# Performance work log

Hardware: AMD Instinct MI355X
Metric: run time of the kernel (lower is better)

The kernel has to match this reference:

```python
import jax, jax.numpy as jnp
import numpy as np

B, T, H = 4, 4096, 1024


def setup_inputs() -> dict:
    key = jax.random.key(0)
    ks = jax.random.split(key, 10)
    W_STD = 0.02  # small init keeps the WKV denominator well-conditioned
    inp = {
        "x": jax.random.normal(ks[0], (B, T, H), dtype=jnp.float32),
        "time_decay": jnp.exp(-jax.random.uniform(ks[1], (H,), minval=0.5, maxval=1.5)),
        "time_mix_key": jax.random.uniform(ks[2], (H,)),
        "time_mix_value": jax.random.uniform(ks[3], (H,)),
        "time_mix_receptance": jax.random.uniform(ks[4], (H,)),
        "W_receptance": jax.random.normal(ks[5], (H, H)) * W_STD,
        "W_key": jax.random.normal(ks[6], (H, H)) * W_STD,
        "W_value": jax.random.normal(ks[7], (H, H)) * W_STD,
        "W_out": jax.random.normal(ks[8], (H, H)) * W_STD,
        "b_out": jax.random.normal(ks[9], (H,)) * W_STD,
    }
    return inp


def reference(x, time_decay, time_mix_key, time_mix_value, time_mix_receptance,
              W_receptance, W_key, W_value, W_out, b_out):
    # time_shift: shifted[:, t] = x[:, t-1], shifted[:, 0] = 0
    shifted = jnp.pad(x, ((0, 0), (1, 0), (0, 0)))[:, :-1]
    xs = x + shifted  # original applies SAME mix to x and shifted
    k = (xs * time_mix_key) @ W_key.T          # [B,T,H]
    v = (xs * time_mix_value) @ W_value.T      # [B,T,H]
    r = jax.nn.sigmoid((xs * time_mix_receptance) @ W_receptance.T)

    def step(carry, kv):
        num, den = carry                       # [B,H] each
        ck, cv = kv                            # [B,H]
        out = (num + time_decay * ck * den) / (den + time_decay * ck)
        ek = jnp.exp(ck)
        return (time_decay * num + ek * cv, time_decay * den + ek), out

    init = (jnp.ones_like(k[:, 0]), jnp.ones_like(k[:, 0]))
    kT = jnp.swapaxes(k, 0, 1)  # [T,B,H]
    vT = jnp.swapaxes(v, 0, 1)
    _, outT = jax.lax.scan(step, init, (kT, vT))
    out = jnp.swapaxes(outT, 0, 1)             # [B,T,H]
    return (r * out) @ W_out.T + b_out
```

## Files before the change

### kernel.cpp

```cpp
#include <hip/hip_runtime.h>

#define H_DIM 1024
#define T_DIM 4096
#define B_DIM 4
#define M_DIM (B_DIM * T_DIM)
#define SCAN_C 32
#define SCAN_W 48

typedef __attribute__((ext_vector_type(8))) short short8;
typedef __attribute__((ext_vector_type(4))) float f32x4;
typedef _Float16 half8 __attribute__((ext_vector_type(8)));

__device__ __forceinline__ unsigned short f2h(float f) {
  _Float16 h = (_Float16)f;
  return __builtin_bit_cast(unsigned short, h);
}
__device__ __forceinline__ float h2f(unsigned short u) {
  return (float)__builtin_bit_cast(_Float16, u);
}

__device__ __forceinline__ double fast_exp64(double x) {
  const double L2E = 1.4426950408889634074;
  const double LN2 = 0.69314718055994530942;
  double z = x * L2E;
  double n = rint(z);
  double y = (z - n) * LN2;
  double p = 2.7557319223985890653e-6;
  p = fma(p, y, 2.4801587301587301566e-5);
  p = fma(p, y, 1.9841269841269841253e-4);
  p = fma(p, y, 1.3888888888888889419e-3);
  p = fma(p, y, 8.3333333333333332177e-3);
  p = fma(p, y, 4.1666666666666664354e-2);
  p = fma(p, y, 1.6666666666666665741e-1);
  p = fma(p, y, 0.5);
  p = fma(p, y, 1.0);
  p = fma(p, y, 1.0);
  long long bits = ((long long)(1023 + (int)n)) << 52;
  return p * __longlong_as_double(bits);
}

__global__ void prep_kernel(const float* __restrict__ x,
                            const float* __restrict__ Wrec, const float* __restrict__ Wkey,
                            const float* __restrict__ Wval, const float* __restrict__ Wout,
                            const float* __restrict__ tmk, const float* __restrict__ tmv,
                            const float* __restrict__ tmr,
                            unsigned short* __restrict__ xs1, unsigned short* __restrict__ xs2,
                            unsigned short* __restrict__ WK1H, unsigned short* __restrict__ WK2H,
                            unsigned short* __restrict__ WVRH, unsigned short* __restrict__ WOH) {
  int bid = blockIdx.x;
  if (bid < 16384) {
    int i = bid * 256 + threadIdx.x;
    const int HV = H_DIM / 4;
    int m = i / HV;
    int t = m & (T_DIM - 1);
    float4 cur = reinterpret_cast<const float4*>(x)[i];
    float4 prev = make_float4(0.f, 0.f, 0.f, 0.f);
    if (t > 0) prev = reinterpret_cast<const float4*>(x)[i - HV];
    float s[4] = {cur.x + prev.x, cur.y + prev.y, cur.z + prev.z, cur.w + prev.w};
    unsigned short a1[4], a2[4];
#pragma unroll
    for (int q = 0; q < 4; ++q) {
      unsigned short h1 = f2h(s[q]);
      a1[q] = h1;
      a2[q] = f2h((s[q] - h2f(h1)) * 2048.0f);
    }
    reinterpret_cast<ushort4*>(xs1)[i] = make_ushort4(a1[0], a1[1], a1[2], a1[3]);
    reinterpret_cast<ushort4*>(xs2)[i] = make_ushort4(a2[0], a2[1], a2[2], a2[3]);
  } else {
    int i = (bid - 16384) * 256 + threadIdx.x;
    int j = i & (H_DIM - 1);
    float wk = Wkey[i] * tmk[j];
    unsigned short k1 = f2h(wk);
    WK1H[i] = k1;
    WK2H[i] = f2h((wk - h2f(k1)) * 2048.0f);
    WVRH[i] = f2h(Wval[i] * tmv[j]);
    WVRH[H_DIM * H_DIM + i] = f2h(Wrec[i] * tmr[j]);
    WOH[i] = f2h(Wout[i]);
  }
}

#define GBAR() do { asm volatile("" ::: "memory"); __builtin_amdgcn_sched_barrier(0); \
                    __builtin_amdgcn_s_barrier(); \
                    __builtin_amdgcn_sched_barrier(0); asm volatile("" ::: "memory"); } while (0)
#define WAIT_VM6() asm volatile("s_waitcnt vmcnt(6)" ::: "memory")
#define WAIT_VM3() asm volatile("s_waitcnt vmcnt(3)" ::: "memory")
#define WAIT_VM0() asm volatile("s_waitcnt vmcnt(0)" ::: "memory")

__device__ __forceinline__ f32x4 mma_h(short8 a, short8 b, f32x4 c) {
  return __builtin_amdgcn_mfma_f32_16x16x32_f16(
      __builtin_bit_cast(half8, a), __builtin_bit_cast(half8, b), c, 0, 0, 0);
}

__device__ __forceinline__ void stage_r128(const unsigned short* base, int rowoff, int kt,
                                           unsigned dst, int wid, int lane,
                                           unsigned char* smem) {
  int row = wid * 16 + (lane >> 2);
  int col8 = (lane & 3) ^ ((row >> 1) & 3);
  const unsigned short* src = base + (size_t)(rowoff + row) * 1024 + kt * 32 + col8 * 8;
  __builtin_amdgcn_global_load_lds(
      (const __attribute__((address_space(1))) void*)src,
      (__attribute__((address_space(3))) void*)(smem + dst + wid * 1024), 16, 0, 0);
}
__device__ __forceinline__ void stage_r256(const unsigned short* base, int rowoff, int kt,
                                           unsigned dst, int wid, int lane,
                                           unsigned char* smem) {
#pragma unroll
  for (int i = 0; i < 2; ++i) {
    int row = wid * 32 + i * 16 + (lane >> 2);
    int col8 = (lane & 3) ^ ((row >> 1) & 3);
    const unsigned short* src = base + (size_t)(rowoff + row) * 1024 + kt * 32 + col8 * 8;
    __builtin_amdgcn_global_load_lds(
        (const __attribute__((address_space(1))) void*)src,
        (__attribute__((address_space(3))) void*)(smem + dst + wid * 2048 + i * 1024), 16, 0, 0);
  }
}
__device__ __forceinline__ short8 frag_ld2(const unsigned char* smem, unsigned rbase,
                                           int row, int kg) {
  return *reinterpret_cast<const short8*>(smem + rbase + row * 64 + ((kg ^ ((row >> 1) & 3)) * 16));
}

__device__ void gemm_k_body(const unsigned short* __restrict__ A1,
                            const unsigned short* __restrict__ A2,
                            const unsigned short* __restrict__ B1,
                            const unsigned short* __restrict__ B2,
                            float* __restrict__ C, int bid, unsigned char* smem) {
  const int tid = threadIdx.x;
  const int wid = tid >> 6;
  const int lane = tid & 63;
  const int wm = wid >> 2;
  const int wn = wid & 3;
  const int frow = lane & 15;
  const int kg = lane >> 4;
  const int swz = (bid & 7) * 64 + (bid >> 3);
  const int brow = (swz >> 2) << 7;
  const int bcol = (swz & 3) << 8;

  f32x4 acc0[4][4], acc1[4][4];
#pragma unroll
  for (int f = 0; f < 4; ++f)
#pragma unroll
    for (int c = 0; c < 4; ++c) {
      acc0[f][c] = (f32x4){0.f, 0.f, 0.f, 0.f};
      acc1[f][c] = (f32x4){0.f, 0.f, 0.f, 0.f};
    }

  const int NT = 32;
#pragma unroll
  for (int t0 = 0; t0 < 2; ++t0) {
    unsigned sb = t0 * 49152u;
    stage_r128(A1, brow, t0, sb + 0u, wid, lane, smem);
    stage_r128(A2, brow, t0, sb + 8192u, wid, lane, smem);
    stage_r256(B1, bcol, t0, sb + 16384u, wid, lane, smem);
    stage_r256(B2, bcol, t0, sb + 32768u, wid, lane, smem);
  }
  WAIT_VM6();
  GBAR();

  for (int t = 0; t < NT; ++t) {
    unsigned sb = (unsigned)(t % 3) * 49152u;
    unsigned st = (unsigned)((t + 2) % 3) * 49152u;
    const bool stg = (t + 2 < NT);
    short8 a1[4], a2[4], b1[4], b2[4];
#pragma unroll
    for (int f = 0; f < 4; ++f) a1[f] = frag_ld2(smem, sb + 0u, wm * 64 + f * 16 + frow, kg);
#pragma unroll
    for (int c = 0; c < 4; ++c) b1[c] = frag_ld2(smem, sb + 16384u, wn * 64 + c * 16 + frow, kg);
    if (stg) {
      stage_r128(A1, brow, t + 2, st + 0u, wid, lane, smem);
      stage_r128(A2, brow, t + 2, st + 8192u, wid, lane, smem);
    }
    GBAR();
    __builtin_amdgcn_s_setprio(1);
#pragma unroll
    for (int f = 0; f < 4; ++f)
#pragma unroll
      for (int c = 0; c < 4; ++c)
        acc0[f][c] = mma_h(a1[f], b1[c], acc0[f][c]);
    __builtin_amdgcn_s_setprio(0);
    GBAR();
#pragma unroll
    for (int c = 0; c < 4; ++c) b2[c] = frag_ld2(smem, sb + 32768u, wn * 64 + c * 16 + frow, kg);
#pragma unroll
    for (int f = 0; f < 4; ++f) a2[f] = frag_ld2(smem, sb + 8192u, wm * 64 + f * 16 + frow, kg);
    if (stg) {
      stage_r256(B1, bcol, t + 2, st + 16384u, wid, lane, smem);
      stage_r256(B2, bcol, t + 2, st + 32768u, wid, lane, smem);
      WAIT_VM6();
    } else {
      WAIT_VM0();
    }
    GBAR();
    __builtin_amdgcn_s_setprio(1);
#pragma unroll
    for (int f = 0; f < 4; ++f)
#pragma unroll
      for (int c = 0; c < 4; ++c)
        acc1[f][c] = mma_h(a1[f], b2[c], acc1[f][c]);
#pragma unroll
    for (int f = 0; f < 4; ++f)
#pragma unroll
      for (int c = 0; c < 4; ++c)
        acc1[f][c] = mma_h(a2[f], b1[c], acc1[f][c]);
    __builtin_amdgcn_s_setprio(0);
    GBAR();
  }
  WAIT_VM0();

#pragma unroll
  for (int f = 0; f < 4; ++f) {
    int r0 = brow + wm * 64 + f * 16 + kg * 4;
#pragma unroll
    for (int c = 0; c < 4; ++c) {
      int cc = bcol + wn * 64 + c * 16 + frow;
#pragma unroll
      for (int q = 0; q < 4; ++q)
        C[(size_t)(r0 + q) * H_DIM + cc] =
            fmaf(0.00048828125f, acc1[f][c][q], acc0[f][c][q]);
    }
  }
}

__device__ __forceinline__ void stage_half(const unsigned short* base, int rowoff,
                                           int ktp, int kk, int slot,
                                           int wid, int lane, unsigned char* smem) {
#pragma unroll
  for (int i = 0; i < 2; ++i) {
    int row = wid * 32 + i * 16 + (lane >> 2);
    int kcol8 = (lane & 3) ^ ((row >> 1) & 3);
    const unsigned short* src = base + (size_t)(rowoff + row) * 1024
                                + ktp * 64 + kk * 32 + kcol8 * 8;
    unsigned int doff = (unsigned int)(slot * 16384 + wid * 2048 + i * 1024);
    __builtin_amdgcn_global_load_lds(
        (const __attribute__((address_space(1))) void*)src,
        (__attribute__((address_space(3))) void*)(smem + doff), 16, 0, 0);
  }
}
__device__ __forceinline__ short8 frag_ld(const unsigned char* smem, int slot, int row, int kg) {
  int byte = slot * 16384 + row * 64 + ((kg ^ ((row >> 1) & 3)) * 16);
  return *reinterpret_cast<const short8*>(smem + byte);
}

__device__ void gemm_vr_body(const unsigned short* __restrict__ Ag,
                             const unsigned short* __restrict__ Bg,
                             unsigned short* __restrict__ C, int bid,
                             unsigned char* smem) {
  const int tid = threadIdx.x;
  const int wid = tid >> 6;
  const int lane = tid & 63;
  const int wm = wid >> 2;
  const int wn = wid & 3;
  const int frow = lane & 15;
  const int kg = lane >> 4;
  const int swz = (bid & 7) * 64 + (bid >> 3);
  const int brow = (swz >> 3) << 8;
  const int bcol = (swz & 7) << 8;

  f32x4 acc[8][4];
#pragma unroll
  for (int f = 0; f < 8; ++f)
#pragma unroll
    for (int c = 0; c < 4; ++c)
      acc[f][c] = (f32x4){0.f, 0.f, 0.f, 0.f};

  const int NT = 16;
  stage_half(Ag, brow, 0, 0, 0, wid, lane, smem);
  stage_half(Bg, bcol, 0, 0, 1, wid, lane, smem);
  stage_half(Ag, brow, 0, 1, 2, wid, lane, smem);
  stage_half(Bg, bcol, 0, 1, 3, wid, lane, smem);
  stage_half(Ag, brow, 1, 0, 4, wid, lane, smem);
  stage_half(Bg, bcol, 1, 0, 5, wid, lane, smem);
  stage_half(Ag, brow, 1, 1, 6, wid, lane, smem);
  WAIT_VM6();
  GBAR();

  for (int t = 0; t < NT; ++t) {
    const int cur4 = (t & 1) * 4;
    const int nxt4 = cur4 ^ 4;
    short8 a[4], b[4];
#pragma unroll
    for (int f = 0; f < 4; ++f) a[f] = frag_ld(smem, cur4 + 0, wm * 128 + f * 16 + frow, kg);
#pragma unroll
    for (int c = 0; c < 4; ++c) b[c] = frag_ld(smem, cur4 + 1, wn * 64 + c * 16 + frow, kg);
    if (t + 1 < NT) stage_half(Bg, bcol, t + 1, 1, nxt4 + 3, wid, lane, smem);
    GBAR();
    __builtin_amdgcn_s_setprio(1);
#pragma unroll
    for (int f = 0; f < 4; ++f)
#pragma unroll
      for (int c = 0; c < 4; ++c)
        acc[f][c] = mma_h(a[f], b[c], acc[f][c]);
    __builtin_amdgcn_s_setprio(0);
    GBAR();
#pragma unroll
    for (int f = 0; f < 4; ++f) a[f] = frag_ld(smem, cur4 + 0, wm * 128 + (f + 4) * 16 + frow, kg);
    if (t + 2 < NT) stage_half(Ag, brow, t + 2, 0, cur4 + 0, wid, lane, smem);
    GBAR();
    __builtin_amdgcn_s_setprio(1);
#pragma unroll
    for (int f = 0; f < 4; ++f)
#pragma unroll
      for (int c = 0; c < 4; ++c)
        acc[f + 4][c] = mma_h(a[f], b[c], acc[f + 4][c]);
    __builtin_amdgcn_s_setprio(0);
    GBAR();
#pragma unroll
    for (int f = 0; f < 4; ++f) a[f] = frag_ld(smem, cur4 + 2, wm * 128 + f * 16 + frow, kg);
#pragma unroll
    for (int c = 0; c < 4; ++c) b[c] = frag_ld(smem, cur4 + 3, wn * 64 + c * 16 + frow, kg);
    if (t + 2 < NT) stage_half(Bg, bcol, t + 2, 0, cur4 + 1, wid, lane, smem);
    GBAR();
    __builtin_amdgcn_s_setprio(1);
#pragma unroll
    for (int f = 0; f < 4; ++f)
#pragma unroll
      for (int c = 0; c < 4; ++c)
        acc[f][c] = mma_h(a[f], b[c], acc[f][c]);
    __builtin_amdgcn_s_setprio(0);
    GBAR();
#pragma unroll
    for (int f = 0; f < 4; ++f) a[f] = frag_ld(smem, cur4 + 2, wm * 128 + (f + 4) * 16 + frow, kg);
    if (t + 2 < NT) stage_half(Ag, brow, t + 2, 1, cur4 + 2, wid, lane, smem);
    if (t + 2 < NT) { WAIT_VM6(); } else { WAIT_VM0(); }
    GBAR();
    __builtin_amdgcn_s_setprio(1);
#pragma unroll
    for (int f = 0; f < 4; ++f)
#pragma unroll
      for (int c = 0; c < 4; ++c)
        acc[f + 4][c] = mma_h(a[f], b[c], acc[f + 4][c]);
    __builtin_amdgcn_s_setprio(0);
    GBAR();
  }
  WAIT_VM0();

#pragma unroll
  for (int f = 0; f < 8; ++f) {
    int r0 = brow + wm * 128 + f * 16 + kg * 4;
#pragma unroll
    for (int c = 0; c < 4; ++c) {
      int cc = bcol + wn * 64 + c * 16 + frow;
#pragma unroll
      for (int q = 0; q < 4; ++q)
        C[(size_t)(r0 + q) * 2048 + cc] = f2h(acc[f][c][q]);
    }
  }
}

__global__ __launch_bounds__(512, 2) void front_kernel(
    const unsigned short* __restrict__ XS1, const unsigned short* __restrict__ XS2,
    const unsigned short* __restrict__ WK1, const unsigned short* __restrict__ WK2,
    const unsigned short* __restrict__ WVR,
    float* __restrict__ Ck, unsigned short* __restrict__ Cvr) {
  __shared__ __attribute__((aligned(16))) unsigned char smem[147456];
  int bid = blockIdx.x;
  if (bid < 512)
    gemm_k_body(XS1, XS2, WK1, WK2, Ck, bid, smem);
  else
    gemm_vr_body(XS1, WVR, Cvr, bid - 512, smem);
}

__global__ __launch_bounds__(512, 4) void gemm_o_kernel(const unsigned short* __restrict__ Ag,
                                                        const unsigned short* __restrict__ Bg,
                                                        float* __restrict__ C,
                                                        const float* __restrict__ bias) {
  __shared__ __attribute__((aligned(16))) unsigned char smem[73728];
  const int tid = threadIdx.x;
  const int wid = tid >> 6;
  const int lane = tid & 63;
  const int wm = wid >> 2;
  const int wn = wid & 3;
  const int frow = lane & 15;
  const int kg = lane >> 4;
  const int bid = blockIdx.x;
  const int swz = (bid & 7) * 64 + (bid >> 3);
  const int brow = (swz >> 2) << 7;
  const int bcol = (swz & 3) << 8;

  f32x4 acc[4][4];
#pragma unroll
  for (int f = 0; f < 4; ++f)
#pragma unroll
    for (int c = 0; c < 4; ++c)
      acc[f][c] = (f32x4){0.f, 0.f, 0.f, 0.f};

  const int NT = 32;
#pragma unroll
  for (int t0 = 0; t0 < 2; ++t0) {
    unsigned sb = t0 * 24576u;
    stage_r128(Ag, brow, t0, sb + 0u, wid, lane, smem);
    stage_r256(Bg, bcol, t0, sb + 8192u, wid, lane, smem);
  }
  WAIT_VM3();
  GBAR();

  for (int t = 0; t < NT; ++t) {
    unsigned sb = (unsigned)(t % 3) * 24576u;
    unsigned st = (unsigned)((t + 2) % 3) * 24576u;
    const bool stg = (t + 2 < NT);
    short8 a[4], b[4];
#pragma unroll
    for (int f = 0; f < 4; ++f) a[f] = frag_ld2(smem, sb + 0u, wm * 64 + f * 16 + frow, kg);
#pragma unroll
    for (int c = 0; c < 4; ++c) b[c] = frag_ld2(smem, sb + 8192u, wn * 64 + c * 16 + frow, kg);
    if (stg) {
      stage_r128(Ag, brow, t + 2, st + 0u, wid, lane, smem);
      stage_r256(Bg, bcol, t + 2, st + 8192u, wid, lane, smem);
      WAIT_VM3();
    } else {
      WAIT_VM0();
    }
    GBAR();
    __builtin_amdgcn_s_setprio(1);
#pragma unroll
    for (int f = 0; f < 4; ++f)
#pragma unroll
      for (int c = 0; c < 4; ++c)
        acc[f][c] = mma_h(a[f], b[c], acc[f][c]);
    __builtin_amdgcn_s_setprio(0);
    GBAR();
  }
  WAIT_VM0();

#pragma unroll
  for (int f = 0; f < 4; ++f) {
    int r0 = brow + wm * 64 + f * 16 + kg * 4;
#pragma unroll
    for (int c = 0; c < 4; ++c) {
      int cc = bcol + wn * 64 + c * 16 + frow;
      float bb = bias[cc];
#pragma unroll
      for (int q = 0; q < 4; ++q)
        C[(size_t)(r0 + q) * H_DIM + cc] = acc[f][c][q] + bb;
    }
  }
}

__global__ void wkv_scan_kernel(const float* __restrict__ kbuf,
                                const unsigned short* __restrict__ vrbuf,
                                const float* __restrict__ tdec,
                                unsigned short* __restrict__ rwh) {
  const int h = (blockIdx.x * 64 + threadIdx.x) * 2;
  const int chunk = blockIdx.y;
  const int b = blockIdx.z;
  const int t0 = chunk * SCAN_C;
  int tstart = t0 - SCAN_W;
  if (tstart < 0) tstart = 0;
  const int tend = t0 + SCAN_C;
  double num0, den0, num1, den1;
  if (tstart == 0) { num0 = num1 = 1.0; den0 = den1 = 1.0; }
  else             { num0 = num1 = 0.0; den0 = den1 = 0.0; }
  const double w0 = (double)tdec[h];
  const double w1 = (double)tdec[h + 1];
  size_t ik = ((size_t)b * T_DIM + tstart) * H_DIM + h;
  size_t iv = ((size_t)b * T_DIM + tstart) * 2048 + h;
  float2 kc = *reinterpret_cast<const float2*>(kbuf + ik);
  unsigned int vc = *reinterpret_cast<const unsigned int*>(vrbuf + iv);
  unsigned int rc = *reinterpret_cast<const unsigned int*>(vrbuf + iv + 1024);
  for (int t = tstart; t < tend; ++t) {
    size_t adv = (t + 1 < tend) ? 1 : 0;
    float2 kn = *reinterpret_cast<const float2*>(kbuf + ik + adv * H_DIM);
    unsigned int vn = *reinterpret_cast<const unsigned int*>(vrbuf + iv + adv * 2048);
    unsigned int rn = *reinterpret_cast<const unsigned int*>(vrbuf + iv + adv * 2048 + 1024);
    double ck0 = (double)kc.x, ck1 = (double)kc.y;
    if (t >= t0) {
      double p0 = w0 * ck0, p1 = w1 * ck1;
      float o0 = (float)fma(p0, den0, num0) / (float)(den0 + p0);
      float o1 = (float)fma(p1, den1, num1) / (float)(den1 + p1);
      float rr0 = 1.0f / (1.0f + __expf(-h2f((unsigned short)(rc & 0xffffu))));
      float rr1 = 1.0f / (1.0f + __expf(-h2f((unsigned short)(rc >> 16))));
      unsigned int wout = (unsigned int)f2h(rr0 * o0) | ((unsigned int)f2h(rr1 * o1) << 16);
      *reinterpret_cast<unsigned int*>(rwh + ik) = wout;
    }
    double ek0 = fast_exp64(ck0);
    double ek1 = fast_exp64(ck1);
    num0 = fma(w0, num0, ek0 * (double)h2f((unsigned short)(vc & 0xffffu)));
    den0 = fma(w0, den0, ek0);
    num1 = fma(w1, num1, ek1 * (double)h2f((unsigned short)(vc >> 16)));
    den1 = fma(w1, den1, ek1);
    kc = kn; vc = vn; rc = rn;
    ik += H_DIM; iv += 2048;
  }
}

extern "C" void kernel_launch(void* const* d_in, const int* in_sizes, int n_in,
                              void* d_out, int out_size, void* d_ws, size_t ws_size,
                              hipStream_t stream) {
  const float* x    = (const float*)d_in[0];
  const float* tdec = (const float*)d_in[1];
  const float* tmk  = (const float*)d_in[2];
  const float* tmv  = (const float*)d_in[3];
  const float* tmr  = (const float*)d_in[4];
  const float* Wrec = (const float*)d_in[5];
  const float* Wkey = (const float*)d_in[6];
  const float* Wval = (const float*)d_in[7];
  const float* Wout = (const float*)d_in[8];
  const float* bout = (const float*)d_in[9];
  float* out = (float*)d_out;
  unsigned char* ws = (unsigned char*)d_ws;

  const size_t W2 = (size_t)H_DIM * H_DIM * 2;
  const size_t BF_FULL = (size_t)M_DIM * H_DIM * 2;
  const size_t NEED = 2 * BF_FULL + 2 * BF_FULL + 5 * W2;
  if (ws_size < NEED) return;

  size_t off = 0;
  unsigned short* XS1H = (unsigned short*)(ws + off); off += BF_FULL;
  unsigned short* XS2H = (unsigned short*)(ws + off); off += BF_FULL;
  unsigned short* VR   = (unsigned short*)(ws + off); off += 2 * BF_FULL;
  unsigned short* WK1H = (unsigned short*)(ws + off); off += W2;
  unsigned short* WK2H = (unsigned short*)(ws + off); off += W2;
  unsigned short* WVRH = (unsigned short*)(ws + off); off += 2 * W2;
  unsigned short* WOH  = (unsigned short*)(ws + off); off += W2;

  prep_kernel<<<dim3(16384 + 4096), dim3(256), 0, stream>>>(
      x, Wrec, Wkey, Wval, Wout, tmk, tmv, tmr, XS1H, XS2H, WK1H, WK2H, WVRH, WOH);

  front_kernel<<<dim3(1024), dim3(512), 0, stream>>>(
      XS1H, XS2H, WK1H, WK2H, WVRH, out, VR);

  unsigned short* RWH = XS1H;
  wkv_scan_kernel<<<dim3(H_DIM / 128, T_DIM / SCAN_C, B_DIM), dim3(64), 0, stream>>>(
      out, VR, tdec, RWH);

  gemm_o_kernel<<<dim3(512), dim3(512), 0, stream>>>(RWH, WOH, out, bout);
}
```

Measured before the change: 305.7 us.

## Retile GEMMs to 256x256, reorder front MFMA phases, float exp in scan

The output GEMM moves from 128x256 to 256x256 tiles with a 3-stage ring of 32 KB stages, and grid and launch bounds are halved to match. The VR GEMM drops its half-k staging for the same triple-buffered 256-row scheme. The front kernel loads b2 earlier so the a1*b2 MFMAs run in the first phase. The scan doubles its chunk size, which cuts redundant warmup over the lookback window, and replaces the double-precision exp polynomial with float __expf. Together these aim to raise data reuse and lower scan ALU cost, at the price of more LDS and register pressure and lower occupancy.

Measured after the change: 303.9 us. No clear change (-0.6%).

```diff
diff --git a/kernel.cpp b/kernel.cpp
--- a/kernel.cpp
+++ b/kernel.cpp
@@ -4,7 +4,7 @@
 #define T_DIM 4096
 #define B_DIM 4
 #define M_DIM (B_DIM * T_DIM)
-#define SCAN_C 32
+#define SCAN_C 64
 #define SCAN_W 48
 
 typedef __attribute__((ext_vector_type(8))) short short8;
@@ -17,26 +17,6 @@
 }
 __device__ __forceinline__ float h2f(unsigned short u) {
   return (float)__builtin_bit_cast(_Float16, u);
-}
-
-__device__ __forceinline__ double fast_exp64(double x) {
-  const double L2E = 1.4426950408889634074;
-  const double LN2 = 0.69314718055994530942;
-  double z = x * L2E;
-  double n = rint(z);
-  double y = (z - n) * LN2;
-  double p = 2.7557319223985890653e-6;
-  p = fma(p, y, 2.4801587301587301566e-5);
-  p = fma(p, y, 1.9841269841269841253e-4);
-  p = fma(p, y, 1.3888888888888889419e-3);
-  p = fma(p, y, 8.3333333333333332177e-3);
-  p = fma(p, y, 4.1666666666666664354e-2);
-  p = fma(p, y, 1.6666666666666665741e-1);
-  p = fma(p, y, 0.5);
-  p = fma(p, y, 1.0);
-  p = fma(p, y, 1.0);
-  long long bits = ((long long)(1023 + (int)n)) << 52;
-  return p * __longlong_as_double(bits);
 }
 
 __global__ void prep_kernel(const float* __restrict__ x,
@@ -83,7 +63,7 @@
                     __builtin_amdgcn_s_barrier(); \
                     __builtin_amdgcn_sched_barrier(0); asm volatile("" ::: "memory"); } while (0)
 #define WAIT_VM6() asm volatile("s_waitcnt vmcnt(6)" ::: "memory")
-#define WAIT_VM3() asm volatile("s_waitcnt vmcnt(3)" ::: "memory")
+#define WAIT_VM4() asm volatile("s_waitcnt vmcnt(4)" ::: "memory")
 #define WAIT_VM0() asm volatile("s_waitcnt vmcnt(0)" ::: "memory")
 
 __device__ __forceinline__ f32x4 mma_h(short8 a, short8 b, f32x4 c) {
@@ -165,6 +145,8 @@
     for (int f = 0; f < 4; ++f) a1[f] = frag_ld2(smem, sb + 0u, wm * 64 + f * 16 + frow, kg);
 #pragma unroll
     for (int c = 0; c < 4; ++c) b1[c] = frag_ld2(smem, sb + 16384u, wn * 64 + c * 16 + frow, kg);
+#pragma unroll
+    for (int c = 0; c < 4; ++c) b2[c] = frag_ld2(smem, sb + 32768u, wn * 64 + c * 16 + frow, kg);
     if (stg) {
       stage_r128(A1, brow, t + 2, st + 0u, wid, lane, smem);
       stage_r128(A2, brow, t + 2, st + 8192u, wid, lane, smem);
@@ -176,10 +158,13 @@
 #pragma unroll
       for (int c = 0; c < 4; ++c)
         acc0[f][c] = mma_h(a1[f], b1[c], acc0[f][c]);
-    __builtin_amdgcn_s_setprio(0);
-    GBAR();
-#pragma unroll
-    for (int c = 0; c < 4; ++c) b2[c] = frag_ld2(smem, sb + 32768u, wn * 64 + c * 16 + frow, kg);
+#pragma unroll
+    for (int f = 0; f < 4; ++f)
+#pragma unroll
+      for (int c = 0; c < 4; ++c)
+        acc1[f][c] = mma_h(a1[f], b2[c], acc1[f][c]);
+    __builtin_amdgcn_s_setprio(0);
+    GBAR();
 #pragma unroll
     for (int f = 0; f < 4; ++f) a2[f] = frag_ld2(smem, sb + 8192u, wm * 64 + f * 16 + frow, kg);
     if (stg) {
@@ -195,11 +180,6 @@
     for (int f = 0; f < 4; ++f)
 #pragma unroll
       for (int c = 0; c < 4; ++c)
-        acc1[f][c] = mma_h(a1[f], b2[c], acc1[f][c]);
-#pragma unroll
-    for (int f = 0; f < 4; ++f)
-#pragma unroll
-      for (int c = 0; c < 4; ++c)
         acc1[f][c] = mma_h(a2[f], b1[c], acc1[f][c]);
     __builtin_amdgcn_s_setprio(0);
     GBAR();
@@ -218,26 +198,6 @@
             fmaf(0.00048828125f, acc1[f][c][q], acc0[f][c][q]);
     }
   }
-}
-
-__device__ __forceinline__ void stage_half(const unsigned short* base, int rowoff,
-                                           int ktp, int kk, int slot,
-                                           int wid, int lane, unsigned char* smem) {
-#pragma unroll
-  for (int i = 0; i < 2; ++i) {
-    int row = wid * 32 + i * 16 + (lane >> 2);
-    int kcol8 = (lane & 3) ^ ((row >> 1) & 3);
-    const unsigned short* src = base + (size_t)(rowoff + row) * 1024
-                                + ktp * 64 + kk * 32 + kcol8 * 8;
-    unsigned int doff = (unsigned int)(slot * 16384 + wid * 2048 + i * 1024);
-    __builtin_amdgcn_global_load_lds(
-        (const __attribute__((address_space(1))) void*)src,
-        (__attribute__((address_space(3))) void*)(smem + doff), 16, 0, 0);
-  }
-}
-__device__ __forceinline__ short8 frag_ld(const unsigned char* smem, int slot, int row, int kg) {
-  int byte = slot * 16384 + row * 64 + ((kg ^ ((row >> 1) & 3)) * 16);
-  return *reinterpret_cast<const short8*>(smem + byte);
 }
 
 __device__ void gemm_vr_body(const unsigned short* __restrict__ Ag,
@@ -262,26 +222,26 @@
     for (int c = 0; c < 4; ++c)
       acc[f][c] = (f32x4){0.f, 0.f, 0.f, 0.f};
 
-  const int NT = 16;
-  stage_half(Ag, brow, 0, 0, 0, wid, lane, smem);
-  stage_half(Bg, bcol, 0, 0, 1, wid, lane, smem);
-  stage_half(Ag, brow, 0, 1, 2, wid, lane, smem);
-  stage_half(Bg, bcol, 0, 1, 3, wid, lane, smem);
-  stage_half(Ag, brow, 1, 0, 4, wid, lane, smem);
-  stage_half(Bg, bcol, 1, 0, 5, wid, lane, smem);
-  stage_half(Ag, brow, 1, 1, 6, wid, lane, smem);
-  WAIT_VM6();
+  const int NT = 32;
+#pragma unroll
+  for (int t0 = 0; t0 < 2; ++t0) {
+    unsigned sb = t0 * 32768u;
+    stage_r256(Ag, brow, t0, sb + 0u, wid, lane, smem);
+    stage_r256(Bg, bcol, t0, sb + 16384u, wid, lane, smem);
+  }
+  WAIT_VM4();
   GBAR();
 
   for (int t = 0; t < NT; ++t) {
-    const int cur4 = (t & 1) * 4;
-    const int nxt4 = cur4 ^ 4;
+    unsigned sb = (unsigned)(t % 3) * 32768u;
+    unsigned st = (unsigned)((t + 2) % 3) * 32768u;
+    const bool stg = (t + 2 < NT);
     short8 a[4], b[4];
 #pragma unroll
-    for (int f = 0; f < 4; ++f) a[f] = frag_ld(smem, cur4 + 0, wm * 128 + f * 16 + frow, kg);
-#pragma unroll
-    for (int c = 0; c < 4; ++c) b[c] = frag_ld(smem, cur4 + 1, wn * 64 + c * 16 + frow, kg);
-    if (t + 1 < NT) stage_half(Bg, bcol, t + 1, 1, nxt4 + 3, wid, lane, smem);
+    for (int f = 0; f < 4; ++f) a[f] = frag_ld2(smem, sb + 0u, wm * 128 + f * 16 + frow, kg);
+#pragma unroll
+    for (int c = 0; c < 4; ++c) b[c] = frag_ld2(smem, sb + 16384u, wn * 64 + c * 16 + frow, kg);
+    if (stg) stage_r256(Ag, brow, t + 2, st + 0u, wid, lane, smem);
     GBAR();
     __builtin_amdgcn_s_setprio(1);
 #pragma unroll
@@ -292,35 +252,13 @@
     __builtin_amdgcn_s_setprio(0);
     GBAR();
 #pragma unroll
-    for (int f = 0; f < 4; ++f) a[f] = frag_ld(smem, cur4 + 0, wm * 128 + (f + 4) * 16 + frow, kg);
-    if (t + 2 < NT) stage_half(Ag, brow, t + 2, 0, cur4 + 0, wid, lane, smem);
-    GBAR();
-    __builtin_amdgcn_s_setprio(1);
-#pragma unroll
-    for (int f = 0; f < 4; ++f)
-#pragma unroll
-      for (int c = 0; c < 4; ++c)
-        acc[f + 4][c] = mma_h(a[f], b[c], acc[f + 4][c]);
-    __builtin_amdgcn_s_setprio(0);
-    GBAR();
-#pragma unroll
-    for (int f = 0; f < 4; ++f) a[f] = frag_ld(smem, cur4 + 2, wm * 128 + f * 16 + frow, kg);
-#pragma unroll
-    for (int c = 0; c < 4; ++c) b[c] = frag_ld(smem, cur4 + 3, wn * 64 + c * 16 + frow, kg);
-    if (t + 2 < NT) stage_half(Bg, bcol, t + 2, 0, cur4 + 1, wid, lane, smem);
-    GBAR();
-    __builtin_amdgcn_s_setprio(1);
-#pragma unroll
-    for (int f = 0; f < 4; ++f)
-#pragma unroll
-      for (int c = 0; c < 4; ++c)
-        acc[f][c] = mma_h(a[f], b[c], acc[f][c]);
-    __builtin_amdgcn_s_setprio(0);
-    GBAR();
-#pragma unroll
-    for (int f = 0; f < 4; ++f) a[f] = frag_ld(smem, cur4 + 2, wm * 128 + (f + 4) * 16 + frow, kg);
-    if (t + 2 < NT) stage_half(Ag, brow, t + 2, 1, cur4 + 2, wid, lane, smem);
-    if (t + 2 < NT) { WAIT_VM6(); } else { WAIT_VM0(); }
+    for (int f = 0; f < 4; ++f) a[f] = frag_ld2(smem, sb + 0u, wm * 128 + (f + 4) * 16 + frow, kg);
+    if (stg) {
+      stage_r256(Bg, bcol, t + 2, st + 16384u, wid, lane, smem);
+      WAIT_VM4();
+    } else {
+      WAIT_VM0();
+    }
     GBAR();
     __builtin_amdgcn_s_setprio(1);
 #pragma unroll
@@ -359,11 +297,11 @@
     gemm_vr_body(XS1, WVR, Cvr, bid - 512, smem);
 }
 
-__global__ __launch_bounds__(512, 4) void gemm_o_kernel(const unsigned short* __restrict__ Ag,
+__global__ __launch_bounds__(512, 2) void gemm_o_kernel(const unsigned short* __restrict__ Ag,
                                                         const unsigned short* __restrict__ Bg,
                                                         float* __restrict__ C,
                                                         const float* __restrict__ bias) {
-  __shared__ __attribute__((aligned(16))) unsigned char smem[73728];
+  __shared__ __attribute__((aligned(16))) unsigned char smem[98304];
   const int tid = threadIdx.x;
   const int wid = tid >> 6;
   const int lane = tid & 63;
@@ -372,13 +310,13 @@
   const int frow = lane & 15;
   const int kg = lane >> 4;
   const int bid = blockIdx.x;
-  const int swz = (bid & 7) * 64 + (bid >> 3);
-  const int brow = (swz >> 2) << 7;
+  const int swz = (bid & 7) * 32 + (bid >> 3);
+  const int brow = (swz >> 2) << 8;
   const int bcol = (swz & 3) << 8;
 
-  f32x4 acc[4][4];
-#pragma unroll
-  for (int f = 0; f < 4; ++f)
+  f32x4 acc[8][4];
+#pragma unroll
+  for (int f = 0; f < 8; ++f)
 #pragma unroll
     for (int c = 0; c < 4; ++c)
       acc[f][c] = (f32x4){0.f, 0.f, 0.f, 0.f};
@@ -386,26 +324,37 @@
   const int NT = 32;
 #pragma unroll
   for (int t0 = 0; t0 < 2; ++t0) {
-    unsigned sb = t0 * 24576u;
-    stage_r128(Ag, brow, t0, sb + 0u, wid, lane, smem);
-    stage_r256(Bg, bcol, t0, sb + 8192u, wid, lane, smem);
-  }
-  WAIT_VM3();
+    unsigned sb = t0 * 32768u;
+    stage_r256(Ag, brow, t0, sb + 0u, wid, lane, smem);
+    stage_r256(Bg, bcol, t0, sb + 16384u, wid, lane, smem);
+  }
+  WAIT_VM4();
   GBAR();
 
   for (int t = 0; t < NT; ++t) {
-    unsigned sb = (unsigned)(t % 3) * 24576u;
-    unsigned st = (unsigned)((t + 2) % 3) * 24576u;
+    unsigned sb = (unsigned)(t % 3) * 32768u;
+    unsigned st = (unsigned)((t + 2) % 3) * 32768u;
     const bool stg = (t + 2 < NT);
     short8 a[4], b[4];
 #pragma unroll
-    for (int f = 0; f < 4; ++f) a[f] = frag_ld2(smem, sb + 0u, wm * 64 + f * 16 + frow, kg);
-#pragma unroll
-    for (int c = 0; c < 4; ++c) b[c] = frag_ld2(smem, sb + 8192u, wn * 64 + c * 16 + frow, kg);
+    for (int f = 0; f < 4; ++f) a[f] = frag_ld2(smem, sb + 0u, wm * 128 + f * 16 + frow, kg);
+#pragma unroll
+    for (int c = 0; c < 4; ++c) b[c] = frag_ld2(smem, sb + 16384u, wn * 64 + c * 16 + frow, kg);
+    if (stg) stage_r256(Ag, brow, t + 2, st + 0u, wid, lane, smem);
+    GBAR();
+    __builtin_amdgcn_s_setprio(1);
+#pragma unroll
+    for (int f = 0; f < 4; ++f)
+#pragma unroll
+      for (int c = 0; c < 4; ++c)
+        acc[f][c] = mma_h(a[f], b[c], acc[f][c]);
+    __builtin_amdgcn_s_setprio(0);
+    GBAR();
+#pragma unroll
+    for (int f = 0; f < 4; ++f) a[f] = frag_ld2(smem, sb + 0u, wm * 128 + (f + 4) * 16 + frow, kg);
     if (stg) {
-      stage_r128(Ag, brow, t + 2, st + 0u, wid, lane, smem);
-      stage_r256(Bg, bcol, t + 2, st + 8192u, wid, lane, smem);
-      WAIT_VM3();
+      stage_r256(Bg, bcol, t + 2, st + 16384u, wid, lane, smem);
+      WAIT_VM4();
     } else {
       WAIT_VM0();
     }
@@ -415,15 +364,15 @@
     for (int f = 0; f < 4; ++f)
 #pragma unroll
       for (int c = 0; c < 4; ++c)
-        acc[f][c] = mma_h(a[f], b[c], acc[f][c]);
+        acc[f + 4][c] = mma_h(a[f], b[c], acc[f + 4][c]);
     __builtin_amdgcn_s_setprio(0);
     GBAR();
   }
   WAIT_VM0();
 
 #pragma unroll
-  for (int f = 0; f < 4; ++f) {
-    int r0 = brow + wm * 64 + f * 16 + kg * 4;
+  for (int f = 0; f < 8; ++f) {
+    int r0 = brow + wm * 128 + f * 16 + kg * 4;
 #pragma unroll
     for (int c = 0; c < 4; ++c) {
       int cc = bcol + wn * 64 + c * 16 + frow;
@@ -461,9 +410,8 @@
     float2 kn = *reinterpret_cast<const float2*>(kbuf + ik + adv * H_DIM);
     unsigned int vn = *reinterpret_cast<const unsigned int*>(vrbuf + iv + adv * 2048);
     unsigned int rn = *reinterpret_cast<const unsigned int*>(vrbuf + iv + adv * 2048 + 1024);
-    double ck0 = (double)kc.x, ck1 = (double)kc.y;
     if (t >= t0) {
-      double p0 = w0 * ck0, p1 = w1 * ck1;
+      double p0 = w0 * (double)kc.x, p1 = w1 * (double)kc.y;
       float o0 = (float)fma(p0, den0, num0) / (float)(den0 + p0);
       float o1 = (float)fma(p1, den1, num1) / (float)(den1 + p1);
       float rr0 = 1.0f / (1.0f + __expf(-h2f((unsigned short)(rc & 0xffffu))));
@@ -471,12 +419,12 @@
       unsigned int wout = (unsigned int)f2h(rr0 * o0) | ((unsigned int)f2h(rr1 * o1) << 16);
       *reinterpret_cast<unsigned int*>(rwh + ik) = wout;
     }
-    double ek0 = fast_exp64(ck0);
-    double ek1 = fast_exp64(ck1);
-    num0 = fma(w0, num0, ek0 * (double)h2f((unsigned short)(vc & 0xffffu)));
-    den0 = fma(w0, den0, ek0);
-    num1 = fma(w1, num1, ek1 * (double)h2f((unsigned short)(vc >> 16)));
-    den1 = fma(w1, den1, ek1);
+    float ek0f = __expf(kc.x);
+    float ek1f = __expf(kc.y);
+    num0 = fma(w0, num0, (double)(ek0f * h2f((unsigned short)(vc & 0xffffu))));
+    den0 = fma(w0, den0, (double)ek0f);
+    num1 = fma(w1, num1, (double)(ek1f * h2f((unsigned short)(vc >> 16))));
+    den1 = fma(w1, den1, (double)ek1f);
     kc = kn; vc = vn; rc = rn;
     ik += H_DIM; iv += 2048;
   }
@@ -522,5 +470,5 @@
   wkv_scan_kernel<<<dim3(H_DIM / 128, T_DIM / SCAN_C, B_DIM), dim3(64), 0, stream>>>(
       out, VR, tdec, RWH);
 
-  gemm_o_kernel<<<dim3(512), dim3(512), 0, stream>>>(RWH, WOH, out, bout);
-}
+  gemm_o_kernel<<<dim3(256), dim3(512), 0, stream>>>(RWH, WOH, out, bout);
+}
```
